# Optimization experiments

Hardware: AMD Instinct MI355X
Metric: run time of the kernel (lower is better)

The kernel has to match this reference:

```python
import jax, jax.numpy as jnp
import numpy as np


def setup_inputs() -> dict:
    key = jax.random.key(0)
    k1, k2, k3, k4 = jax.random.split(key, 4)
    B, C, H, W = 8, 256, 64, 64
    x = jax.random.normal(k1, (B, C, H, W), dtype=jnp.float32)
    wq = jax.random.normal(k2, (1, C), dtype=jnp.float32) * (1.0 / np.sqrt(C))
    wk = jax.random.normal(k3, (1, C), dtype=jnp.float32) * (1.0 / np.sqrt(C))
    wv = jax.random.normal(k4, (C, C), dtype=jnp.float32) * (1.0 / np.sqrt(C))
    gamma = jnp.zeros((1,), dtype=jnp.float32)
    return {"x": x, "wq": wq, "wk": wk, "wv": wv, "gamma": gamma}


def reference(x, wq, wk, wv, gamma):
    B, C, H, W = x.shape
    N = H * W
    xf = x.reshape(B, C, N)                      # [B, C, N]
    # 1x1 convs == channel matmuls
    f = jnp.einsum('oc,bcn->bon', wq, xf)        # [B, 1, N]
    g = jnp.einsum('oc,bcn->bon', wk, xf)        # [B, 1, N]
    h = jnp.einsum('oc,bcn->bon', wv, xf)        # [B, C, N]
    # scores[b, i, j] = f[b, 0, i] * g[b, 0, j]  -> [B, N, N]
    scores = jnp.einsum('bi,bj->bij', f[:, 0, :], g[:, 0, :])
    # softmax over dim=1 (rows), matching torch F.softmax(..., dim=1)
    beta = jax.nn.softmax(scores, axis=1)        # [B, N, N]
    gam = gamma[0]
    o = (1.0 - gam) * jnp.einsum('bcn,bnm->bcm', h, beta) + gam * xf
    return o.reshape(B, C, H, W)
```

## Files before the change

### kernel.cpp

```cpp
#include <hip/hip_runtime.h>
#include <math.h>

#define BQ 8
#define CQ 256
#define NQ 4096
#define MT 64
#define NCH 128

typedef short s16x8 __attribute__((ext_vector_type(8)));
typedef short s16x4 __attribute__((ext_vector_type(4)));
typedef float f32x4 __attribute__((ext_vector_type(4)));
typedef unsigned int uint;

static __device__ __forceinline__ float4 ld4(const float* p) { return *(const float4*)p; }

static constexpr float LOG2E = 1.4426950408889634f;

static __device__ __forceinline__ short f2bf(float f) {
    return __builtin_bit_cast(short, (__bf16)f);
}
static __device__ __forceinline__ uint fkey(float f) {
    uint b = __builtin_bit_cast(uint, f);
    return b ^ (0x80000000u | (uint)((int)b >> 31));
}
static __device__ __forceinline__ float fdec(uint u) {
    uint b = (u & 0x80000000u) ? (u ^ 0x80000000u) : ~u;
    return __builtin_bit_cast(float, b);
}

__global__ void k_fg(const float* __restrict__ x, const float* __restrict__ wq,
                     const float* __restrict__ wk, float* __restrict__ fs,
                     float* __restrict__ g, short* __restrict__ xbf,
                     uint* __restrict__ fmxu, uint* __restrict__ fmnu) {
    int b = blockIdx.y;
    int t = threadIdx.x;
    int nl = (t & 31) * 2;
    int cg = t >> 5;
    int n = blockIdx.x * 64 + nl;
    const float* xb = x + (size_t)b * CQ * NQ + n;
    uint* xo = (uint*)(xbf + (size_t)b * CQ * NQ + n);
    float f0 = 0.f, f1 = 0.f, g0 = 0.f, g1 = 0.f;
    int c0 = cg * 32;
#pragma unroll 8
    for (int c = c0; c < c0 + 32; ++c) {
        float2 v = *(const float2*)&xb[(size_t)c * NQ];
        f0 = fmaf(wq[c], v.x, f0);
        f1 = fmaf(wq[c], v.y, f1);
        g0 = fmaf(wk[c], v.x, g0);
        g1 = fmaf(wk[c], v.y, g1);
        uint p = (uint)(unsigned short)f2bf(v.x) | ((uint)(unsigned short)f2bf(v.y) << 16);
        xo[c * (NQ / 2)] = p;
    }
    __shared__ float sf[8][64], sg2[8][64];
    sf[cg][nl] = f0;  sf[cg][nl + 1] = f1;
    sg2[cg][nl] = g0; sg2[cg][nl + 1] = g1;
    __syncthreads();
    if (t < 64) {
        float f = 0.f, gg = 0.f;
#pragma unroll
        for (int i = 0; i < 8; ++i) { f += sf[i][t]; gg += sg2[i][t]; }
        f *= LOG2E;
        fs[b * NQ + blockIdx.x * 64 + t] = f;
        g[b * NQ + blockIdx.x * 64 + t]  = gg;
        float mx = f, mn = f;
#pragma unroll
        for (int off = 32; off; off >>= 1) {
            mx = fmaxf(mx, __shfl_xor(mx, off));
            mn = fminf(mn, __shfl_xor(mn, off));
        }
        if (t == 0) {
            atomicMax(&fmxu[b], fkey(mx));
            atomicMin(&fmnu[b], fkey(mn));
        }
    }
}

#define EOFF 32768
#define ESLOT 5120
#define ZOFF 43008
#define SMEM_BYTES 44032

#define STAGE(slot, ch)                                                            \
    {                                                                              \
        _Pragma("unroll")                                                          \
        for (int i_ = 0; i_ < 2; ++i_) {                                           \
            int off_ = tid * 16 + i_ * 8192;                                       \
            int row_ = off_ >> 6, nb_ = off_ & 63;                                 \
            const short* src_ = xb + (size_t)row_ * NQ + (ch) * 32 + (nb_ >> 1);   \
            __builtin_amdgcn_global_load_lds(                                      \
                (const __attribute__((address_space(1))) void*)src_,               \
                (__attribute__((address_space(3))) void*)(smem + (slot) * 16384 + off_), \
                16, 0, 0);                                                         \
        }                                                                          \
    }

__global__ void __launch_bounds__(512, 4) k_attn(
    const short* __restrict__ xbf, const float* __restrict__ fsp,
    const float* __restrict__ gp, const uint* __restrict__ fmxu,
    const uint* __restrict__ fmnu, const float* __restrict__ wv,
    const float* __restrict__ x, const float* __restrict__ gamma,
    float* __restrict__ out) {
    __shared__ __align__(16) char smem[SMEM_BYTES];

    int bid = blockIdx.x;
    int b = bid & 7;
    int mblk = bid >> 3;
    int m0 = mblk * MT;
    int tid = threadIdx.x;
    int l = tid & 63;
    int w = tid >> 6;
    int q = l >> 4;
    int cr = l & 15;

    const short* xb = xbf + (size_t)b * CQ * NQ;
    const float* fb = fsp + b * NQ;

    STAGE(0, 0)

    int wc = w >> 1;
    int wm = w & 1;
    f32x4 acc[8][2];
#pragma unroll
    for (int jc = 0; jc < 8; ++jc)
#pragma unroll
        for (int jm = 0; jm < 2; ++jm) acc[jc][jm] = (f32x4){0.f, 0.f, 0.f, 0.f};

    int p = w - 4;
    float gv = 0.f, nM = 0.f, zac = 0.f;
    float4 fca = {0,0,0,0}, fcb = {0,0,0,0}, fna = {0,0,0,0}, fnb = {0,0,0,0};

    if (w >= 4) {
        float fmx = fdec(fmxu[b]), fmn = fdec(fmnu[b]);
        gv = gp[b * NQ + m0 + l];
        nM = -((gv >= 0.f) ? gv * fmx : gv * fmn);
        float4 a0 = ld4(fb + p * 8);
        float4 b0 = ld4(fb + p * 8 + 4);
        float fq[8] = {a0.x, a0.y, a0.z, a0.w, b0.x, b0.y, b0.z, b0.w};
        s16x8 ev;
#pragma unroll
        for (int i = 0; i < 8; ++i) {
            float e = __builtin_amdgcn_exp2f(fmaf(fq[i], gv, nM));
            zac += e;
            ev[i] = f2bf(e);
        }
        *(s16x8*)(smem + EOFF + l * 80 + p * 16) = ev;
        fca = ld4(fb + 32 + p * 8);  fcb = ld4(fb + 32 + p * 8 + 4);
        fna = ld4(fb + 64 + p * 8);  fnb = ld4(fb + 64 + p * 8 + 4);
    }
    __syncthreads();

    for (int s = 0; s < NCH; ++s) {
        if (s + 1 < NCH) STAGE((s + 1) & 1, s + 1)
        if (w < 4) {
            const char* cbuf = smem + (s & 1) * 16384;
            const char* ebuf = smem + EOFF + (s & 1) * ESLOT;
            s16x8 bv0 = *(const s16x8*)(ebuf + (wm * 32 + cr) * 80 + q * 16);
            s16x8 bv1 = *(const s16x8*)(ebuf + (wm * 32 + 16 + cr) * 80 + q * 16);
#pragma unroll
            for (int jc = 0; jc < 8; ++jc) {
                s16x8 av = *(const s16x8*)(cbuf + (wc * 128 + jc * 16 + cr) * 64 + q * 16);
                acc[jc][0] = __builtin_amdgcn_mfma_f32_16x16x32_bf16(av, bv0, acc[jc][0], 0, 0, 0);
                acc[jc][1] = __builtin_amdgcn_mfma_f32_16x16x32_bf16(av, bv1, acc[jc][1], 0, 0, 0);
            }
        } else if (s + 1 < NCH) {
            float fq[8] = {fca.x, fca.y, fca.z, fca.w, fcb.x, fcb.y, fcb.z, fcb.w};
            s16x8 ev;
#pragma unroll
            for (int i = 0; i < 8; ++i) {
                float e = __builtin_amdgcn_exp2f(fmaf(fq[i], gv, nM));
                zac += e;
                ev[i] = f2bf(e);
            }
            *(s16x8*)(smem + EOFF + ((s + 1) & 1) * ESLOT + l * 80 + p * 16) = ev;
            fca = fna; fcb = fnb;
            int ch = (s + 3) & (NCH - 1);
            fna = ld4(fb + ch * 32 + p * 8);
            fnb = ld4(fb + ch * 32 + p * 8 + 4);
        }
        __syncthreads();
    }

    if (w >= 4) ((float*)(smem + ZOFF))[p * 64 + l] = zac;
    __syncthreads();

    if (w < 4) {
        const float* zb = (const float*)(smem + ZOFF);
        float rzl[2];
#pragma unroll
        for (int jm = 0; jm < 2; ++jm) {
            int mloc = wm * 32 + jm * 16 + cr;
            float z = zb[mloc] + zb[64 + mloc] + zb[128 + mloc] + zb[192 + mloc];
            rzl[jm] = 1.0f / z;
        }
#pragma unroll
        for (int jc = 0; jc < 8; ++jc) {
#pragma unroll
            for (int jm = 0; jm < 2; ++jm) {
                int mloc = wm * 32 + jm * 16 + cr;
                int cb = (wc * 256 + jc * 32 + q * 8) ^ ((mloc & 7) << 4);
                s16x4 v;
#pragma unroll
                for (int r = 0; r < 4; ++r) v[r] = f2bf(acc[jc][jm][r] * rzl[jm]);
                *(s16x4*)(smem + mloc * 512 + cb) = v;
            }
        }
    }
    __syncthreads();

    int co0 = w * 32;
    f32x4 acc2[2][4];
#pragma unroll
    for (int j2 = 0; j2 < 2; ++j2)
#pragma unroll
        for (int jm2 = 0; jm2 < 4; ++jm2) acc2[j2][jm2] = (f32x4){0.f, 0.f, 0.f, 0.f};

#pragma unroll 2
    for (int ks = 0; ks < 8; ++ks) {
        s16x8 a2[2];
#pragma unroll
        for (int j2 = 0; j2 < 2; ++j2) {
            const float* wr = wv + (size_t)(co0 + j2 * 16 + cr) * CQ + ks * 32 + q * 8;
            float4 wa = ld4(wr);
            float4 wb = ld4(wr + 4);
            a2[j2][0] = f2bf(wa.x); a2[j2][1] = f2bf(wa.y);
            a2[j2][2] = f2bf(wa.z); a2[j2][3] = f2bf(wa.w);
            a2[j2][4] = f2bf(wb.x); a2[j2][5] = f2bf(wb.y);
            a2[j2][6] = f2bf(wb.z); a2[j2][7] = f2bf(wb.w);
        }
#pragma unroll
        for (int jm2 = 0; jm2 < 4; ++jm2) {
            int mloc = jm2 * 16 + cr;
            s16x8 b2 = *(const s16x8*)(smem + mloc * 512 + ((ks * 64 + q * 16) ^ ((mloc & 7) << 4)));
#pragma unroll
            for (int j2 = 0; j2 < 2; ++j2)
                acc2[j2][jm2] = __builtin_amdgcn_mfma_f32_16x16x32_bf16(a2[j2], b2, acc2[j2][jm2], 0, 0, 0);
        }
    }

    float gam = gamma[0];
    float omg = 1.f - gam;
    if (gam != 0.f) {
#pragma unroll
        for (int j2 = 0; j2 < 2; ++j2)
#pragma unroll
            for (int jm2 = 0; jm2 < 4; ++jm2)
#pragma unroll
                for (int r = 0; r < 4; ++r) {
                    int c_out = co0 + j2 * 16 + q * 4 + r;
                    size_t idx = ((size_t)b * CQ + c_out) * NQ + m0 + jm2 * 16 + cr;
                    __builtin_nontemporal_store(
                        fmaf(gam, x[idx], acc2[j2][jm2][r] * omg), out + idx);
                }
    } else {
#pragma unroll
        for (int j2 = 0; j2 < 2; ++j2)
#pragma unroll
            for (int jm2 = 0; jm2 < 4; ++jm2)
#pragma unroll
                for (int r = 0; r < 4; ++r) {
                    int c_out = co0 + j2 * 16 + q * 4 + r;
                    size_t idx = ((size_t)b * CQ + c_out) * NQ + m0 + jm2 * 16 + cr;
                    __builtin_nontemporal_store(acc2[j2][jm2][r] * omg, out + idx);
                }
    }
}

extern "C" void kernel_launch(void* const* d_in, const int* in_sizes, int n_in,
                              void* d_out, int out_size, void* d_ws, size_t ws_size,
                              hipStream_t stream) {
    const float* x     = (const float*)d_in[0];
    const float* wq    = (const float*)d_in[1];
    const float* wk    = (const float*)d_in[2];
    const float* wv    = (const float*)d_in[3];
    const float* gamma = (const float*)d_in[4];
    float* out = (float*)d_out;

    float* ws  = (float*)d_ws;
    float* fs  = ws;
    float* g   = ws + BQ * NQ;
    uint* fmxu = (uint*)(ws + 2 * BQ * NQ);
    uint* fmnu = fmxu + 8;
    short* xbf = (short*)(ws + 2 * BQ * NQ + 64);

    hipMemsetAsync(fmxu, 0x00, 32, stream);
    hipMemsetAsync(fmnu, 0xFF, 32, stream);
    hipLaunchKernelGGL(k_fg, dim3(NQ / 64, BQ), dim3(256), 0, stream,
                       x, wq, wk, fs, g, xbf, fmxu, fmnu);
    hipLaunchKernelGGL(k_attn, dim3(BQ * (NQ / MT)), dim3(512), 0, stream,
                       xbf, fs, g, fmxu, fmnu, wv, x, gamma, out);
}
```

Measured before the change: 137.4 us.

## Double attention output tile to 128 columns with XOR-swizzled LDS layout

Each block now handles 128 output positions instead of 64, so every staged bf16 chunk of x is reused across twice as many MFMAs. This halves the number of blocks and the total global/LDS traffic for x. The exp-producer warps compute two rows each, and the x and exp tiles in LDS use an XOR swizzle instead of padding to avoid bank conflicts. In exchange, the accumulator count per thread doubles, LDS grows, launch bounds drop to 2 blocks per CU, and the grid shrinks to 256 blocks, which may underfill the GPU.

```diff
diff --git a/kernel.cpp b/kernel.cpp
--- a/kernel.cpp
+++ b/kernel.cpp
@@ -4,7 +4,7 @@
 #define BQ 8
 #define CQ 256
 #define NQ 4096
-#define MT 64
+#define MT 128
 #define NCH 128
 
 typedef short s16x8 __attribute__((ext_vector_type(8)));
@@ -76,17 +76,18 @@
 }
 
 #define EOFF 32768
-#define ESLOT 5120
-#define ZOFF 43008
-#define SMEM_BYTES 44032
+#define ESLOT 8192
+#define ZOFF 65536
+#define SMEM_BYTES 67584
 
 #define STAGE(slot, ch)                                                            \
     {                                                                              \
         _Pragma("unroll")                                                          \
         for (int i_ = 0; i_ < 2; ++i_) {                                           \
             int off_ = tid * 16 + i_ * 8192;                                       \
-            int row_ = off_ >> 6, nb_ = off_ & 63;                                 \
-            const short* src_ = xb + (size_t)row_ * NQ + (ch) * 32 + (nb_ >> 1);   \
+            int row_ = (tid >> 2) + i_ * 128;                                      \
+            int slot_ = (tid & 3) ^ ((row_ >> 1) & 3);                             \
+            const short* src_ = xb + (size_t)row_ * NQ + (ch) * 32 + slot_ * 8;    \
             __builtin_amdgcn_global_load_lds(                                      \
                 (const __attribute__((address_space(1))) void*)src_,               \
                 (__attribute__((address_space(3))) void*)(smem + (slot) * 16384 + off_), \
@@ -94,7 +95,7 @@
         }                                                                          \
     }
 
-__global__ void __launch_bounds__(512, 4) k_attn(
+__global__ void __launch_bounds__(512, 2) k_attn(
     const short* __restrict__ xbf, const float* __restrict__ fsp,
     const float* __restrict__ gp, const uint* __restrict__ fmxu,
     const uint* __restrict__ fmnu, const float* __restrict__ wv,
@@ -111,6 +112,7 @@
     int w = tid >> 6;
     int q = l >> 4;
     int cr = l & 15;
+    int qp16 = (q ^ ((cr >> 1) & 3)) * 16;
 
     const short* xb = xbf + (size_t)b * CQ * NQ;
     const float* fb = fsp + b * NQ;
@@ -119,31 +121,36 @@
 
     int wc = w >> 1;
     int wm = w & 1;
-    f32x4 acc[8][2];
+    f32x4 acc[8][4];
 #pragma unroll
     for (int jc = 0; jc < 8; ++jc)
 #pragma unroll
-        for (int jm = 0; jm < 2; ++jm) acc[jc][jm] = (f32x4){0.f, 0.f, 0.f, 0.f};
+        for (int jm = 0; jm < 4; ++jm) acc[jc][jm] = (f32x4){0.f, 0.f, 0.f, 0.f};
 
     int p = w - 4;
-    float gv = 0.f, nM = 0.f, zac = 0.f;
+    int eslotA = (p ^ ((l >> 1) & 3)) * 16;
+    float gvA = 0.f, gvB = 0.f, nMA = 0.f, nMB = 0.f, zacA = 0.f, zacB = 0.f;
     float4 fca = {0,0,0,0}, fcb = {0,0,0,0}, fna = {0,0,0,0}, fnb = {0,0,0,0};
 
     if (w >= 4) {
         float fmx = fdec(fmxu[b]), fmn = fdec(fmnu[b]);
-        gv = gp[b * NQ + m0 + l];
-        nM = -((gv >= 0.f) ? gv * fmx : gv * fmn);
+        gvA = gp[b * NQ + m0 + l];
+        gvB = gp[b * NQ + m0 + l + 64];
+        nMA = -((gvA >= 0.f) ? gvA * fmx : gvA * fmn);
+        nMB = -((gvB >= 0.f) ? gvB * fmx : gvB * fmn);
         float4 a0 = ld4(fb + p * 8);
         float4 b0 = ld4(fb + p * 8 + 4);
         float fq[8] = {a0.x, a0.y, a0.z, a0.w, b0.x, b0.y, b0.z, b0.w};
-        s16x8 ev;
+        s16x8 evA, evB;
 #pragma unroll
         for (int i = 0; i < 8; ++i) {
-            float e = __builtin_amdgcn_exp2f(fmaf(fq[i], gv, nM));
-            zac += e;
-            ev[i] = f2bf(e);
-        }
-        *(s16x8*)(smem + EOFF + l * 80 + p * 16) = ev;
+            float eA = __builtin_amdgcn_exp2f(fmaf(fq[i], gvA, nMA));
+            float eB = __builtin_amdgcn_exp2f(fmaf(fq[i], gvB, nMB));
+            zacA += eA; zacB += eB;
+            evA[i] = f2bf(eA); evB[i] = f2bf(eB);
+        }
+        *(s16x8*)(smem + EOFF + l * 64 + eslotA) = evA;
+        *(s16x8*)(smem + EOFF + (l + 64) * 64 + eslotA) = evB;
         fca = ld4(fb + 32 + p * 8);  fcb = ld4(fb + 32 + p * 8 + 4);
         fna = ld4(fb + 64 + p * 8);  fnb = ld4(fb + 64 + p * 8 + 4);
     }
@@ -154,24 +161,30 @@
         if (w < 4) {
             const char* cbuf = smem + (s & 1) * 16384;
             const char* ebuf = smem + EOFF + (s & 1) * ESLOT;
-            s16x8 bv0 = *(const s16x8*)(ebuf + (wm * 32 + cr) * 80 + q * 16);
-            s16x8 bv1 = *(const s16x8*)(ebuf + (wm * 32 + 16 + cr) * 80 + q * 16);
+            s16x8 bv[4];
+#pragma unroll
+            for (int jm = 0; jm < 4; ++jm)
+                bv[jm] = *(const s16x8*)(ebuf + (wm * 64 + jm * 16 + cr) * 64 + qp16);
 #pragma unroll
             for (int jc = 0; jc < 8; ++jc) {
-                s16x8 av = *(const s16x8*)(cbuf + (wc * 128 + jc * 16 + cr) * 64 + q * 16);
-                acc[jc][0] = __builtin_amdgcn_mfma_f32_16x16x32_bf16(av, bv0, acc[jc][0], 0, 0, 0);
-                acc[jc][1] = __builtin_amdgcn_mfma_f32_16x16x32_bf16(av, bv1, acc[jc][1], 0, 0, 0);
+                s16x8 av = *(const s16x8*)(cbuf + (wc * 128 + jc * 16 + cr) * 64 + qp16);
+#pragma unroll
+                for (int jm = 0; jm < 4; ++jm)
+                    acc[jc][jm] = __builtin_amdgcn_mfma_f32_16x16x32_bf16(av, bv[jm], acc[jc][jm], 0, 0, 0);
             }
         } else if (s + 1 < NCH) {
+            char* ebuf = smem + EOFF + ((s + 1) & 1) * ESLOT;
             float fq[8] = {fca.x, fca.y, fca.z, fca.w, fcb.x, fcb.y, fcb.z, fcb.w};
-            s16x8 ev;
+            s16x8 evA, evB;
 #pragma unroll
             for (int i = 0; i < 8; ++i) {
-                float e = __builtin_amdgcn_exp2f(fmaf(fq[i], gv, nM));
-                zac += e;
-                ev[i] = f2bf(e);
+                float eA = __builtin_amdgcn_exp2f(fmaf(fq[i], gvA, nMA));
+                float eB = __builtin_amdgcn_exp2f(fmaf(fq[i], gvB, nMB));
+                zacA += eA; zacB += eB;
+                evA[i] = f2bf(eA); evB[i] = f2bf(eB);
             }
-            *(s16x8*)(smem + EOFF + ((s + 1) & 1) * ESLOT + l * 80 + p * 16) = ev;
+            *(s16x8*)(ebuf + l * 64 + eslotA) = evA;
+            *(s16x8*)(ebuf + (l + 64) * 64 + eslotA) = evB;
             fca = fna; fcb = fnb;
             int ch = (s + 3) & (NCH - 1);
             fna = ld4(fb + ch * 32 + p * 8);
@@ -180,23 +193,27 @@
         __syncthreads();
     }
 
-    if (w >= 4) ((float*)(smem + ZOFF))[p * 64 + l] = zac;
+    if (w >= 4) {
+        float* zb = (float*)(smem + ZOFF);
+        zb[p * 128 + l] = zacA;
+        zb[p * 128 + l + 64] = zacB;
+    }
     __syncthreads();
 
     if (w < 4) {
         const float* zb = (const float*)(smem + ZOFF);
-        float rzl[2];
-#pragma unroll
-        for (int jm = 0; jm < 2; ++jm) {
-            int mloc = wm * 32 + jm * 16 + cr;
-            float z = zb[mloc] + zb[64 + mloc] + zb[128 + mloc] + zb[192 + mloc];
+        float rzl[4];
+#pragma unroll
+        for (int jm = 0; jm < 4; ++jm) {
+            int mloc = wm * 64 + jm * 16 + cr;
+            float z = zb[mloc] + zb[128 + mloc] + zb[256 + mloc] + zb[384 + mloc];
             rzl[jm] = 1.0f / z;
         }
 #pragma unroll
         for (int jc = 0; jc < 8; ++jc) {
 #pragma unroll
-            for (int jm = 0; jm < 2; ++jm) {
-                int mloc = wm * 32 + jm * 16 + cr;
+            for (int jm = 0; jm < 4; ++jm) {
+                int mloc = wm * 64 + jm * 16 + cr;
                 int cb = (wc * 256 + jc * 32 + q * 8) ^ ((mloc & 7) << 4);
                 s16x4 v;
 #pragma unroll
@@ -208,11 +225,11 @@
     __syncthreads();
 
     int co0 = w * 32;
-    f32x4 acc2[2][4];
+    f32x4 acc2[2][8];
 #pragma unroll
     for (int j2 = 0; j2 < 2; ++j2)
 #pragma unroll
-        for (int jm2 = 0; jm2 < 4; ++jm2) acc2[j2][jm2] = (f32x4){0.f, 0.f, 0.f, 0.f};
+        for (int jm2 = 0; jm2 < 8; ++jm2) acc2[j2][jm2] = (f32x4){0.f, 0.f, 0.f, 0.f};
 
 #pragma unroll 2
     for (int ks = 0; ks < 8; ++ks) {
@@ -228,7 +245,7 @@
             a2[j2][6] = f2bf(wb.z); a2[j2][7] = f2bf(wb.w);
         }
 #pragma unroll
-        for (int jm2 = 0; jm2 < 4; ++jm2) {
+        for (int jm2 = 0; jm2 < 8; ++jm2) {
             int mloc = jm2 * 16 + cr;
             s16x8 b2 = *(const s16x8*)(smem + mloc * 512 + ((ks * 64 + q * 16) ^ ((mloc & 7) << 4)));
 #pragma unroll
@@ -243,7 +260,7 @@
 #pragma unroll
         for (int j2 = 0; j2 < 2; ++j2)
 #pragma unroll
-            for (int jm2 = 0; jm2 < 4; ++jm2)
+            for (int jm2 = 0; jm2 < 8; ++jm2)
 #pragma unroll
                 for (int r = 0; r < 4; ++r) {
                     int c_out = co0 + j2 * 16 + q * 4 + r;
@@ -255,7 +272,7 @@
 #pragma unroll
         for (int j2 = 0; j2 < 2; ++j2)
 #pragma unroll
-            for (int jm2 = 0; jm2 < 4; ++jm2)
+            for (int jm2 = 0; jm2 < 8; ++jm2)
 #pragma unroll
                 for (int r = 0; r < 4; ++r) {
                     int c_out = co0 + j2 * 16 + q * 4 + r;
```

After: 142.4 us. 1.04x slower.
